# Kernel optimization log

Hardware: AMD Instinct MI355X
Metric: run time of the kernel (lower is better)

Reference implementation:

```python
import jax, jax.numpy as jnp
import numpy as np

D, M, B, K = 512, 128, 16, 4
COHERENCE_COEFF = 0.01
LAMBDA_COEFF = 1.0


def setup_inputs() -> dict:
    key = jax.random.key(0)
    k1, k2, k3, k4 = jax.random.split(key, 4)
    x = jax.random.normal(k1, (2, 2048, D), dtype=jnp.float32)
    V = jax.random.normal(k2, (D, M, B), dtype=jnp.float32)
    U = jax.random.normal(k3, (M, D, B), dtype=jnp.float32)
    u_scales = jax.random.normal(k4, (M, B), dtype=jnp.float32)
    return {"x": x, "V": V, "U": U, "u_scales": u_scales}


def _forward(x, V, U, u_scales):
    # UnitColNorm parametrizations: normalize over the D axis
    Vn = V / jnp.linalg.norm(V, axis=0, keepdims=True)          # (D, m, b)
    Un = U / jnp.linalg.norm(U, axis=1, keepdims=True)          # (m, D, b)
    s = jnp.tanh(u_scales) * LAMBDA_COEFF                        # (m, b)
    U_eff = Un * s[:, None, :]                                   # (m, D, b)

    expert_reprs = jnp.einsum('...d,dmb->...mb', x, Vn)          # (..., m, b)
    repr_l2_sq = jnp.sum(expert_reprs * expert_reprs, axis=-1)   # (..., m)
    topk_vals, topk_idxs = jax.lax.top_k(repr_l2_sq, K)          # (..., k)

    reprs_topk = jnp.take_along_axis(expert_reprs, topk_idxs[..., None], axis=-2)  # (..., k, b)
    U_active = U_eff[topk_idxs]                                  # (..., k, D, b)
    writes = jnp.einsum('...kdb,...kb->...d', U_active, reprs_topk)

    # aux terms
    N = topk_vals.size // K
    idxs_flat = topk_idxs.reshape(-1)
    vals_flat = topk_vals.reshape(-1)
    energy_per_expert = jnp.zeros((M,), dtype=vals_flat.dtype).at[idxs_flat].add(vals_flat) / N
    select_rate = jnp.zeros((M,), dtype=vals_flat.dtype).at[idxs_flat].add(1.0) / N
    total_energy = jnp.maximum(energy_per_expert.sum(), 1e-12)
    relative_energy = energy_per_expert / total_energy

    eye = jnp.eye(M * B, dtype=Vn.dtype)
    sqrtD = jnp.sqrt(jnp.asarray(D, dtype=Vn.dtype))

    def coherence_penalty(Mtx):
        G = Mtx.T @ Mtx  # (m*b, m*b)
        return jnp.abs(G - eye).mean() * sqrtD

    v_pen = coherence_penalty(Vn.reshape(D, M * B))
    u_pen = coherence_penalty(U_eff.transpose(1, 0, 2).reshape(D, M * B))
    aux_loss = COHERENCE_COEFF * v_pen - total_energy

    out = x + writes
    return (out, total_energy, energy_per_expert, relative_energy,
            select_rate, v_pen, u_pen, aux_loss)


def reference(x, V, U, u_scales):
    return _forward(x, V, U, u_scales)
```

## Files before the change

### kernel.cpp

```cpp
#include <hip/hip_runtime.h>
#include <math.h>

#define D 512
#define M 128
#define B 16
#define KSEL 4
#define NC 2048
#define NTOK 4096

typedef unsigned short ushort;
typedef unsigned int uint;
typedef unsigned long long u64;
typedef __attribute__((ext_vector_type(8))) short short8;
typedef __attribute__((ext_vector_type(4))) float floatx4;

#define WS_EACC   0
#define WS_CACC   128
#define WS_VSUM   256
#define WS_USUM   257
#define WS_CNT_I  258
#define WS_VSCALE 512
#define WS_USCALE 2560
#define WS_E_F    4608
#define WS_RBF_F  528896
#define WS_XH_F   2626048
#define WS_XL_F   3674624
#define WS_VHT_F  4723200
#define WS_VLT_F  5247488
#define WS_UHT_F  5771776
#define WS_ULT_F  6296064
#define WS_LIST_F 6820352
#define WS_SEL_F  7344640

#define OUT_TE   2097152
#define OUT_EPE  2097153
#define OUT_RE   2097281
#define OUT_SR   2097409
#define OUT_VPEN 2097537
#define OUT_UPEN 2097538
#define OUT_AUX  2097539

#define GLDS16(g, l) __builtin_amdgcn_global_load_lds(                        \
    (const __attribute__((address_space(1))) unsigned int*)(g),               \
    (__attribute__((address_space(3))) unsigned int*)(l), 16, 0, 0)

__device__ __forceinline__ ushort f2bf(float f) {
    union { float f; uint u; } a; a.f = f;
    uint u = a.u;
    u += 0x7fffu + ((u >> 16) & 1u);
    return (ushort)(u >> 16);
}
__device__ __forceinline__ float bf2f(ushort h) {
    union { uint u; float f; } a; a.u = ((uint)h) << 16;
    return a.f;
}

__launch_bounds__(256)
__global__ void prep_kernel(const float* __restrict__ x, const float* __restrict__ V,
                            const float* __restrict__ U, const float* __restrict__ us_in,
                            ushort* __restrict__ xh, ushort* __restrict__ xl,
                            ushort* __restrict__ vht, ushort* __restrict__ vlt,
                            ushort* __restrict__ uht, ushort* __restrict__ ult,
                            float* __restrict__ ws) {
    __shared__ float ts[64][65];
    const int bid = blockIdx.x;
    const int tid = threadIdx.x;

    if (bid < 1024) {
        const int idx = (bid * 256 + tid) * 8;
        float4 v0 = *(const float4*)(x + idx);
        float4 v1 = *(const float4*)(x + idx + 4);
        float vv[8] = {v0.x, v0.y, v0.z, v0.w, v1.x, v1.y, v1.z, v1.w};
        union { ushort u[8]; uint4 q; } H, L;
#pragma unroll
        for (int j = 0; j < 8; ++j) {
            ushort h = f2bf(vv[j]);
            H.u[j] = h;
            L.u[j] = f2bf(vv[j] - bf2f(h));
        }
        *(uint4*)(xh + idx) = H.q;
        *(uint4*)(xl + idx) = L.q;
    } else if (bid < 1280) {
        const int vb = bid - 1024;
        const int col0 = (vb & 31) * 64;
        const int d0 = (vb >> 5) * 64;
#pragma unroll
        for (int i = 0; i < 16; ++i) {
            int idx = i * 256 + tid;
            int r = idx >> 6, c = idx & 63;
            ts[r][c] = V[(size_t)(d0 + r) * NC + col0 + c];
        }
        __syncthreads();
#pragma unroll
        for (int i = 0; i < 16; ++i) {
            int idx = i * 256 + tid;
            int c2 = idx >> 6, d2 = idx & 63;
            float v = ts[d2][c2];
            ushort h = f2bf(v);
            vht[(size_t)(col0 + c2) * D + d0 + d2] = h;
            vlt[(size_t)(col0 + c2) * D + d0 + d2] = f2bf(v - bf2f(h));
        }
    } else if (bid < 1408) {
        const int m = bid - 1280;
        float (*t2)[129] = (float (*)[129])ts;
        for (int d0 = 0; d0 < D; d0 += 128) {
            __syncthreads();
#pragma unroll
            for (int i = 0; i < 8; ++i) {
                int idx = i * 256 + tid;
                int d2 = idx >> 4, b2 = idx & 15;
                t2[b2][d2] = U[(size_t)m * (D * B) + (size_t)(d0 + d2) * B + b2];
            }
            __syncthreads();
#pragma unroll
            for (int i = 0; i < 8; ++i) {
                int idx = i * 256 + tid;
                int b3 = idx >> 7, d3 = idx & 127;
                uht[(size_t)((m << 4) + b3) * D + d0 + d3] = f2bf(t2[b3][d3]);
            }
        }
    } else {
        const int bx = bid - 1408;
        if (bx >= 160) {
            ws[(bx - 160) * 256 + tid] = 0.0f;
            return;
        }
        if (bx < 32) {
            const int c = bx * 64 + (tid & 63);
            const int dg = tid >> 6;
            float s = 0.0f;
            for (int d = dg; d < D; d += 4) {
                float v = V[(size_t)d * NC + c];
                s = fmaf(v, v, s);
            }
            float (*sh)[64] = (float (*)[64])ts;
            sh[dg][tid & 63] = s;
            __syncthreads();
            if (tid < 64) {
                float t = (sh[0][tid] + sh[1][tid]) + (sh[2][tid] + sh[3][tid]);
                ws[WS_VSCALE + bx * 64 + tid] = 1.0f / sqrtf(t);
            }
        } else {
            const int m = bx - 32;
            const float* p = U + (size_t)m * (D * B);
            float s = 0.0f;
            for (int i = tid; i < D * B; i += 256) {
                float v = p[i];
                s = fmaf(v, v, s);
            }
            float* sh2 = &ts[0][0];
            sh2[tid] = s;
            __syncthreads();
            if (tid < 16) {
                float t = 0.0f;
#pragma unroll
                for (int j = 0; j < 16; ++j) t += sh2[tid + (j << 4)];
                ws[WS_USCALE + (m << 4) + tid] = tanhf(us_in[(m << 4) + tid]) / sqrtf(t);
            }
        }
    }
}

__launch_bounds__(256)
__global__ void mfma_fused(const ushort* __restrict__ xh, const ushort* __restrict__ xl,
                           const ushort* __restrict__ vht, const ushort* __restrict__ vlt,
                           const ushort* __restrict__ uht, const ushort* __restrict__ ult,
                           float* __restrict__ ws, ushort* __restrict__ rbf) {
    __shared__ ushort smem[16384];
    const int bid = blockIdx.x;
    const int tid = threadIdx.x, lane = tid & 63, w = tid >> 6;
    const int wr = w >> 1, wc = w & 1;
    const int r15 = lane & 15, q = lane >> 4;
    const int srl = lane >> 2;
    const int skq = (lane & 3) ^ ((lane >> 3) & 3);
    const int perm8 = (q ^ ((r15 >> 1) & 3)) * 8;

    const int is_gemm = bid < 512;
    const ushort* srcs[4];
    int rbase[4];
    int gi = 0, gj = 0, which = 0;
    if (is_gemm) {
        const int x = bid & 7, inner = bid >> 3;
        const int tokG = ((x >> 1) << 3) + (inner & 7);
        const int colG = ((x & 1) << 3) + (inner >> 3);
        const int tokB = tokG * 128, colB = colG * 128;
        srcs[0] = xh; srcs[1] = xl; srcs[2] = vht; srcs[3] = vlt;
        rbase[0] = tokB; rbase[1] = tokB; rbase[2] = colB; rbase[3] = colB;
    } else {
        int t = bid - 512;
        which = t >= 136;
        if (which) t -= 136;
        int bi = 0, rem = 16;
        while (t >= rem) { t -= rem; --rem; ++bi; }
        gi = bi; gj = bi + t;
        const ushort* ht = which ? uht : vht;
        srcs[0] = ht; srcs[1] = ht; srcs[2] = ht; srcs[3] = ht;
        rbase[0] = gi * 128; rbase[1] = gi * 128; rbase[2] = gj * 128; rbase[3] = gj * 128;
    }

    floatx4 acc[4][4];
#pragma unroll
    for (int i = 0; i < 4; ++i)
#pragma unroll
        for (int j = 0; j < 4; ++j) acc[i][j] = (floatx4){0.f, 0.f, 0.f, 0.f};

    auto stage = [&](int c) {
        const int kb = c * 32 + skq * 8;
#pragma unroll
        for (int tI = 0; tI < 4; ++tI) {
            if (!is_gemm && (tI & 1)) continue;
            const ushort* s = srcs[tI] + (size_t)rbase[tI] * D + kb;
#pragma unroll
            for (int sub = 0; sub < 2; ++sub) {
                const int row16 = w * 32 + sub * 16;
                GLDS16(s + (size_t)(row16 + srl) * D,
                       &smem[tI * 4096 + row16 * 32]);
            }
        }
    };

    stage(0);
    for (int c = 0; c < 16; ++c) {
        __syncthreads();
        short8 ah[4], al[4], bh[4], bl[4];
#pragma unroll
        for (int s = 0; s < 4; ++s) {
            const int ra = (wr * 64 + s * 16 + r15) * 32 + perm8;
            ah[s] = *(const short8*)&smem[ra];
            const int rb = (wc * 64 + s * 16 + r15) * 32 + perm8;
            bh[s] = *(const short8*)&smem[8192 + rb];
            if (is_gemm) {
                al[s] = *(const short8*)&smem[4096 + ra];
                bl[s] = *(const short8*)&smem[12288 + rb];
            }
        }
        __syncthreads();
        if (c < 15) stage(c + 1);
#pragma unroll
        for (int st = 0; st < 4; ++st)
#pragma unroll
            for (int sc = 0; sc < 4; ++sc) {
                acc[st][sc] = __builtin_amdgcn_mfma_f32_16x16x32_bf16(ah[st], bh[sc], acc[st][sc], 0, 0, 0);
                if (is_gemm) {
                    acc[st][sc] = __builtin_amdgcn_mfma_f32_16x16x32_bf16(ah[st], bl[sc], acc[st][sc], 0, 0, 0);
                    acc[st][sc] = __builtin_amdgcn_mfma_f32_16x16x32_bf16(al[st], bh[sc], acc[st][sc], 0, 0, 0);
                }
            }
    }

    if (is_gemm) {
        const int tok0 = rbase[0] + wr * 64, col0 = rbase[2] + wc * 64;
        const int cg4 = col0 >> 6;
        float* e2base = ws + WS_E_F + (size_t)cg4 * (NTOK * 4);
#pragma unroll
        for (int st = 0; st < 4; ++st) {
            const int rowb = tok0 + st * 16 + q * 4;
            float er[4][4];
#pragma unroll
            for (int sc = 0; sc < 4; ++sc) {
                const int colg = col0 + sc * 16 + r15;
                const float vs = ws[WS_VSCALE + colg];
                float r0 = acc[st][sc][0] * vs;
                float r1 = acc[st][sc][1] * vs;
                float r2 = acc[st][sc][2] * vs;
                float r3 = acc[st][sc][3] * vs;
                rbf[(size_t)(rowb + 0) * NC + colg] = f2bf(r0);
                rbf[(size_t)(rowb + 1) * NC + colg] = f2bf(r1);
                rbf[(size_t)(rowb + 2) * NC + colg] = f2bf(r2);
                rbf[(size_t)(rowb + 3) * NC + colg] = f2bf(r3);
                float e0 = r0 * r0, e1 = r1 * r1, e2 = r2 * r2, e3 = r3 * r3;
#pragma unroll
                for (int mk = 1; mk < 16; mk <<= 1) {
                    e0 += __shfl_xor(e0, mk);
                    e1 += __shfl_xor(e1, mk);
                    e2 += __shfl_xor(e2, mk);
                    e3 += __shfl_xor(e3, mk);
                }
                er[sc][0] = e0; er[sc][1] = e1; er[sc][2] = e2; er[sc][3] = e3;
            }
            if (r15 == 0) {
#pragma unroll
                for (int j = 0; j < 4; ++j) {
                    *(float4*)(e2base + (size_t)(rowb + j) * 4) =
                        make_float4(er[0][j], er[1][j], er[2][j], er[3][j]);
                }
            }
        }
    } else {
        const float* scl = ws + (which ? WS_USCALE : WS_VSCALE);
        float* sum_out = ws + (which ? WS_USUM : WS_VSUM);
        float local = 0.0f;
#pragma unroll
        for (int sc = 0; sc < 4; ++sc) {
            const int colg = gj * 128 + wc * 64 + sc * 16 + r15;
            const float scj = scl[colg];
#pragma unroll
            for (int st = 0; st < 4; ++st) {
#pragma unroll
                for (int reg = 0; reg < 4; ++reg) {
                    const int rowg = gi * 128 + wr * 64 + st * 16 + q * 4 + reg;
                    float g = acc[st][sc][reg] * scl[rowg] * scj;
                    if (rowg == colg) g -= 1.0f;
                    local += fabsf(g);
                }
            }
        }
        if (gi < gj) local *= 2.0f;
#pragma unroll
        for (int mk = 1; mk < 64; mk <<= 1) local += __shfl_xor(local, mk);
        __shared__ float red[4];
        if (lane == 0) red[w] = local;
        __syncthreads();
        if (tid == 0) atomicAdd(sum_out, (red[0] + red[1]) + (red[2] + red[3]));
    }
}

__launch_bounds__(256)
__global__ void topk_kernel(float* __restrict__ ws) {
    const int tid = threadIdx.x, lane = tid & 63, w = tid >> 6;
    const int t = blockIdx.x * 4 + w;

    const int cg4 = lane >> 1;
    const int e2off = (lane & 1) * 2;
    const float2 ev = *(const float2*)(ws + WS_E_F +
                                       ((size_t)cg4 * NTOK + t) * 4 + e2off);
    const uint i0 = (uint)(lane * 2), i1 = i0 + 1;
    u64 k0 = ((u64)__float_as_uint(ev.x) << 32) | (uint)(~i0);
    u64 k1 = ((u64)__float_as_uint(ev.y) << 32) | (uint)(~i1);
    u64 s0 = k0 > k1 ? k0 : k1;
    u64 s1 = k0 > k1 ? k1 : k0;
    u64 s2 = 0, s3 = 0;

#pragma unroll
    for (int mk = 1; mk < 64; mk <<= 1) {
        u64 o0 = __shfl_xor(s0, mk);
        u64 o1 = __shfl_xor(s1, mk);
        u64 o2 = __shfl_xor(s2, mk);
        u64 o3 = __shfl_xor(s3, mk);
        u64 c0 = s0 > o3 ? s0 : o3;
        u64 c1 = s1 > o2 ? s1 : o2;
        u64 c2 = s2 > o1 ? s2 : o1;
        u64 c3 = s3 > o0 ? s3 : o0;
        u64 d0 = c0 > c2 ? c0 : c2, d2 = c0 > c2 ? c2 : c0;
        u64 d1 = c1 > c3 ? c1 : c3, d3 = c1 > c3 ? c3 : c1;
        s0 = d0 > d1 ? d0 : d1; s1 = d0 > d1 ? d1 : d0;
        s2 = d2 > d3 ? d2 : d3; s3 = d2 > d3 ? d3 : d2;
    }

    if (lane < 4) {
        u64 key = (lane == 0) ? s0 : (lane == 1) ? s1 : (lane == 2) ? s2 : s3;
        const uint e = (uint)(~(uint)key) & 127u;
        const u64 lo = ((u64)(e << 14)) | (u64)((t << 2) | lane);
        ((u64*)(ws + WS_SEL_F))[(t << 2) + lane] =
            (key & 0xFFFFFFFF00000000ull) | lo;
    }
}

__launch_bounds__(256)
__global__ void listbuild_kernel(float* __restrict__ ws) {
    const int e = blockIdx.x;
    const int tid = threadIdx.x;
    const u64* sels = (const u64*)(ws + WS_SEL_F);
    int* icnt = (int*)ws + WS_CNT_I;
    int* ilist = (int*)(ws + WS_LIST_F) + (e << 12);

    __shared__ int sc_[256];
    __shared__ float sv[256];

    const int base_idx = tid * 64;
    int cnt = 0;
    float vsum = 0.0f;
#pragma unroll 8
    for (int j = 0; j < 64; ++j) {
        u64 s = sels[base_idx + j];
        if ((int)((s >> 14) & 127u) == e) {
            ++cnt;
            vsum += __uint_as_float((uint)(s >> 32));
        }
    }
    sc_[tid] = cnt;
    sv[tid] = vsum;
    __syncthreads();

#pragma unroll
    for (int off = 1; off < 256; off <<= 1) {
        int v = (tid >= off) ? sc_[tid - off] : 0;
        __syncthreads();
        sc_[tid] += v;
        __syncthreads();
    }
    const int wbase = sc_[tid] - cnt;
    const int total = sc_[255];

    if (cnt > 0) {
        int p = wbase;
#pragma unroll 8
        for (int j = 0; j < 64; ++j) {
            u64 s = sels[base_idx + j];
            if ((int)((s >> 14) & 127u) == e)
                ilist[p++] = (int)(s & 0x3FFFu);
        }
    }

#pragma unroll
    for (int off = 128; off > 0; off >>= 1) {
        __syncthreads();
        if (tid < off) sv[tid] += sv[tid + off];
    }
    if (tid == 0) {
        icnt[e] = total;
        ws[WS_EACC + e] = sv[0];
        ws[WS_CACC + e] = (float)total;
    }
}

__launch_bounds__(256)
__global__ void expert_contrib_kernel(const float* __restrict__ U,
                                      const ushort* __restrict__ rbf,
                                      const float* __restrict__ ws,
                                      uint* __restrict__ contrib) {
    const int e = blockIdx.x;
    const int tid = threadIdx.x;
    const int cnt = ((const int*)ws)[WS_CNT_I + e];
    if ((int)blockIdx.y >= cnt) return;

    float usc[16];
#pragma unroll
    for (int b = 0; b < 16; ++b) usc[b] = ws[WS_USCALE + (e << 4) + b];

    const float* Up = U + (size_t)e * (D * B);
    float u0[16], u1[16];
#pragma unroll
    for (int qd = 0; qd < 4; ++qd) {
        float4 a = *(const float4*)(Up + (size_t)(2 * tid) * B + qd * 4);
        float4 b4 = *(const float4*)(Up + (size_t)(2 * tid + 1) * B + qd * 4);
        u0[qd * 4 + 0] = a.x * usc[qd * 4 + 0];
        u0[qd * 4 + 1] = a.y * usc[qd * 4 + 1];
        u0[qd * 4 + 2] = a.z * usc[qd * 4 + 2];
        u0[qd * 4 + 3] = a.w * usc[qd * 4 + 3];
        u1[qd * 4 + 0] = b4.x * usc[qd * 4 + 0];
        u1[qd * 4 + 1] = b4.y * usc[qd * 4 + 1];
        u1[qd * 4 + 2] = b4.z * usc[qd * 4 + 2];
        u1[qd * 4 + 3] = b4.w * usc[qd * 4 + 3];
    }

    const int* ilist = (const int*)(ws + WS_LIST_F) + (e << 12);
    int i = blockIdx.y;
    int pk = (i < cnt) ? ilist[i] : 0;
    while (i < cnt) {
        const int t = pk >> 2, k = pk & 3;
        const ushort* rp = rbf + (size_t)t * NC + (e << 4);
        union { ushort u[16]; uint4 q[2]; } R;
        R.q[0] = *(const uint4*)(rp);
        R.q[1] = *(const uint4*)(rp + 8);
        const int inext = i + 8;
        if (inext < cnt) pk = ilist[inext];
        float acc0 = 0.0f, acc1 = 0.0f;
#pragma unroll
        for (int b = 0; b < 16; ++b) {
            const float wv = bf2f(R.u[b]);
            acc0 = fmaf(u0[b], wv, acc0);
            acc1 = fmaf(u1[b], wv, acc1);
        }
        contrib[(size_t)((t << 2) + k) * 256 + tid] =
            (uint)f2bf(acc0) | ((uint)f2bf(acc1) << 16);
        i = inext;
    }
}

__launch_bounds__(256)
__global__ void combine_kernel(const float* __restrict__ x,
                               const uint* __restrict__ contrib,
                               const float* __restrict__ ws,
                               float* __restrict__ out) {
    if (blockIdx.x == 1024) {
        const int m = threadIdx.x;
        if (m >= 128) return;
        float e = ws[WS_EACC + m] * (1.0f / (float)NTOK);
        float c = ws[WS_CACC + m] * (1.0f / (float)NTOK);
        float s = e;
#pragma unroll
        for (int off = 32; off > 0; off >>= 1) s += __shfl_down(s, off);
        __shared__ float sh[2];
        if ((m & 63) == 0) sh[m >> 6] = s;
        __syncthreads();
        float total = sh[0] + sh[1];
        float total_energy = fmaxf(total, 1e-12f);
        out[OUT_EPE + m] = e;
        out[OUT_RE + m] = e / total_energy;
        out[OUT_SR + m] = c;
        if (m == 0) {
            out[OUT_TE] = total_energy;
            float inv_n2 = 1.0f / ((float)NC * (float)NC);
            float sqrtD = sqrtf((float)D);
            float vpen = ws[WS_VSUM] * inv_n2 * sqrtD;
            float upen = ws[WS_USUM] * inv_n2 * sqrtD;
            out[OUT_VPEN] = vpen;
            out[OUT_UPEN] = upen;
            out[OUT_AUX] = 0.01f * vpen - total_energy;
        }
        return;
    }

    const int gid = blockIdx.x * 256 + threadIdx.x;
    const int t = gid >> 6;
    const int dq = (gid & 63) << 3;
    const uint4* cp = (const uint4*)contrib;

    float s[8];
    float4 x0 = *(const float4*)(x + (size_t)t * D + dq);
    float4 x1 = *(const float4*)(x + (size_t)t * D + dq + 4);
    s[0] = x0.x; s[1] = x0.y; s[2] = x0.z; s[3] = x0.w;
    s[4] = x1.x; s[5] = x1.y; s[6] = x1.z; s[7] = x1.w;
#pragma unroll
    for (int k = 0; k < KSEL; ++k) {
        uint4 cvec = cp[(size_t)((t << 2) + k) * 64 + (dq >> 3)];
        uint cc[4] = {cvec.x, cvec.y, cvec.z, cvec.w};
#pragma unroll
        for (int j = 0; j < 4; ++j) {
            s[2 * j]     += bf2f((ushort)(cc[j] & 0xffffu));
            s[2 * j + 1] += bf2f((ushort)(cc[j] >> 16));
        }
    }
    float* op = out + (size_t)t * D + dq;
    *(float4*)(op)     = make_float4(s[0], s[1], s[2], s[3]);
    *(float4*)(op + 4) = make_float4(s[4], s[5], s[6], s[7]);
}

extern "C" void kernel_launch(void* const* d_in, const int* in_sizes, int n_in,
                              void* d_out, int out_size, void* d_ws, size_t ws_size,
                              hipStream_t stream) {
    const float* x  = (const float*)d_in[0];
    const float* V  = (const float*)d_in[1];
    const float* U  = (const float*)d_in[2];
    const float* us = (const float*)d_in[3];
    float* out = (float*)d_out;
    float* ws  = (float*)d_ws;

    ushort* xh  = (ushort*)(ws + WS_XH_F);
    ushort* xl  = (ushort*)(ws + WS_XL_F);
    ushort* vht = (ushort*)(ws + WS_VHT_F);
    ushort* vlt = (ushort*)(ws + WS_VLT_F);
    ushort* uht = (ushort*)(ws + WS_UHT_F);
    ushort* ult = (ushort*)(ws + WS_ULT_F);
    ushort* rbf = (ushort*)(ws + WS_RBF_F);
    uint* contrib = (uint*)(ws + WS_XH_F);

    prep_kernel<<<1570, 256, 0, stream>>>(x, V, U, us, xh, xl, vht, vlt, uht, ult, ws);
    mfma_fused<<<784, 256, 0, stream>>>(xh, xl, vht, vlt, uht, ult, ws, rbf);
    topk_kernel<<<NTOK / 4, 256, 0, stream>>>(ws);
    listbuild_kernel<<<M, 256, 0, stream>>>(ws);
    expert_contrib_kernel<<<dim3(128, 8), 256, 0, stream>>>(U, rbf, ws, contrib);
    combine_kernel<<<1025, 256, 0, stream>>>(x, contrib, ws, out);
}
```

Before: 168.9 us.

## Fuse topk, list build, expert contrib and combine into one cooperative kernel

The four tail kernels (top-k selection, per-expert list build, expert contribution, final combine) are merged into one cooperatively launched kernel of 1024 blocks, with grid-wide syncs between phases. The aim is to remove the launch gaps and drain/fill bubbles between these small kernels. The cost is three grid barriers. It also requires all 1024 blocks to be co-resident, which `__launch_bounds__(256, 4)` targets. Unused `ult` pointer arguments are dropped from the earlier kernels.

```diff
diff --git a/kernel.cpp b/kernel.cpp
--- a/kernel.cpp
+++ b/kernel.cpp
@@ -1,5 +1,8 @@
 #include <hip/hip_runtime.h>
+#include <hip/hip_cooperative_groups.h>
 #include <math.h>
+
+namespace cg = cooperative_groups;
 
 #define D 512
 #define M 128
@@ -60,7 +63,7 @@
                             const float* __restrict__ U, const float* __restrict__ us_in,
                             ushort* __restrict__ xh, ushort* __restrict__ xl,
                             ushort* __restrict__ vht, ushort* __restrict__ vlt,
-                            ushort* __restrict__ uht, ushort* __restrict__ ult,
+                            ushort* __restrict__ uht,
                             float* __restrict__ ws) {
     __shared__ float ts[64][65];
     const int bid = blockIdx.x;
@@ -164,7 +167,7 @@
 __launch_bounds__(256)
 __global__ void mfma_fused(const ushort* __restrict__ xh, const ushort* __restrict__ xl,
                            const ushort* __restrict__ vht, const ushort* __restrict__ vlt,
-                           const ushort* __restrict__ uht, const ushort* __restrict__ ult,
+                           const ushort* __restrict__ uht,
                            float* __restrict__ ws, ushort* __restrict__ rbf) {
     __shared__ ushort smem[16384];
     const int bid = blockIdx.x;
@@ -315,216 +318,218 @@
     }
 }
 
-__launch_bounds__(256)
-__global__ void topk_kernel(float* __restrict__ ws) {
+__launch_bounds__(256, 4)
+__global__ void tail_kernel(const float* __restrict__ x, const float* __restrict__ U,
+                            const ushort* __restrict__ rbf, float* __restrict__ ws,
+                            uint* __restrict__ contrib, float* __restrict__ out) {
+    cg::grid_group grid = cg::this_grid();
+    const int bid = blockIdx.x;
     const int tid = threadIdx.x, lane = tid & 63, w = tid >> 6;
-    const int t = blockIdx.x * 4 + w;
-
-    const int cg4 = lane >> 1;
-    const int e2off = (lane & 1) * 2;
-    const float2 ev = *(const float2*)(ws + WS_E_F +
-                                       ((size_t)cg4 * NTOK + t) * 4 + e2off);
-    const uint i0 = (uint)(lane * 2), i1 = i0 + 1;
-    u64 k0 = ((u64)__float_as_uint(ev.x) << 32) | (uint)(~i0);
-    u64 k1 = ((u64)__float_as_uint(ev.y) << 32) | (uint)(~i1);
-    u64 s0 = k0 > k1 ? k0 : k1;
-    u64 s1 = k0 > k1 ? k1 : k0;
-    u64 s2 = 0, s3 = 0;
-
-#pragma unroll
-    for (int mk = 1; mk < 64; mk <<= 1) {
-        u64 o0 = __shfl_xor(s0, mk);
-        u64 o1 = __shfl_xor(s1, mk);
-        u64 o2 = __shfl_xor(s2, mk);
-        u64 o3 = __shfl_xor(s3, mk);
-        u64 c0 = s0 > o3 ? s0 : o3;
-        u64 c1 = s1 > o2 ? s1 : o2;
-        u64 c2 = s2 > o1 ? s2 : o1;
-        u64 c3 = s3 > o0 ? s3 : o0;
-        u64 d0 = c0 > c2 ? c0 : c2, d2 = c0 > c2 ? c2 : c0;
-        u64 d1 = c1 > c3 ? c1 : c3, d3 = c1 > c3 ? c3 : c1;
-        s0 = d0 > d1 ? d0 : d1; s1 = d0 > d1 ? d1 : d0;
-        s2 = d2 > d3 ? d2 : d3; s3 = d2 > d3 ? d3 : d2;
-    }
-
-    if (lane < 4) {
-        u64 key = (lane == 0) ? s0 : (lane == 1) ? s1 : (lane == 2) ? s2 : s3;
-        const uint e = (uint)(~(uint)key) & 127u;
-        const u64 lo = ((u64)(e << 14)) | (u64)((t << 2) | lane);
-        ((u64*)(ws + WS_SEL_F))[(t << 2) + lane] =
-            (key & 0xFFFFFFFF00000000ull) | lo;
-    }
-}
-
-__launch_bounds__(256)
-__global__ void listbuild_kernel(float* __restrict__ ws) {
-    const int e = blockIdx.x;
-    const int tid = threadIdx.x;
-    const u64* sels = (const u64*)(ws + WS_SEL_F);
-    int* icnt = (int*)ws + WS_CNT_I;
-    int* ilist = (int*)(ws + WS_LIST_F) + (e << 12);
 
     __shared__ int sc_[256];
     __shared__ float sv[256];
-
-    const int base_idx = tid * 64;
-    int cnt = 0;
-    float vsum = 0.0f;
-#pragma unroll 8
-    for (int j = 0; j < 64; ++j) {
-        u64 s = sels[base_idx + j];
-        if ((int)((s >> 14) & 127u) == e) {
-            ++cnt;
-            vsum += __uint_as_float((uint)(s >> 32));
-        }
-    }
-    sc_[tid] = cnt;
-    sv[tid] = vsum;
-    __syncthreads();
-
-#pragma unroll
-    for (int off = 1; off < 256; off <<= 1) {
-        int v = (tid >= off) ? sc_[tid - off] : 0;
-        __syncthreads();
-        sc_[tid] += v;
-        __syncthreads();
-    }
-    const int wbase = sc_[tid] - cnt;
-    const int total = sc_[255];
-
-    if (cnt > 0) {
-        int p = wbase;
+    __shared__ float sh2[2];
+
+    {
+        const int t = bid * 4 + w;
+        const int cg4 = lane >> 1;
+        const int e2off = (lane & 1) * 2;
+        const float2 ev = *(const float2*)(ws + WS_E_F +
+                                           ((size_t)cg4 * NTOK + t) * 4 + e2off);
+        const uint i0 = (uint)(lane * 2), i1 = i0 + 1;
+        u64 k0 = ((u64)__float_as_uint(ev.x) << 32) | (uint)(~i0);
+        u64 k1 = ((u64)__float_as_uint(ev.y) << 32) | (uint)(~i1);
+        u64 s0 = k0 > k1 ? k0 : k1;
+        u64 s1 = k0 > k1 ? k1 : k0;
+        u64 s2 = 0, s3 = 0;
+
+#pragma unroll
+        for (int mk = 1; mk < 64; mk <<= 1) {
+            u64 o0 = __shfl_xor(s0, mk);
+            u64 o1 = __shfl_xor(s1, mk);
+            u64 o2 = __shfl_xor(s2, mk);
+            u64 o3 = __shfl_xor(s3, mk);
+            u64 c0 = s0 > o3 ? s0 : o3;
+            u64 c1 = s1 > o2 ? s1 : o2;
+            u64 c2 = s2 > o1 ? s2 : o1;
+            u64 c3 = s3 > o0 ? s3 : o0;
+            u64 d0 = c0 > c2 ? c0 : c2, d2 = c0 > c2 ? c2 : c0;
+            u64 d1 = c1 > c3 ? c1 : c3, d3 = c1 > c3 ? c3 : c1;
+            s0 = d0 > d1 ? d0 : d1; s1 = d0 > d1 ? d1 : d0;
+            s2 = d2 > d3 ? d2 : d3; s3 = d2 > d3 ? d3 : d2;
+        }
+
+        if (lane < 4) {
+            u64 key = (lane == 0) ? s0 : (lane == 1) ? s1 : (lane == 2) ? s2 : s3;
+            const uint e = (uint)(~(uint)key) & 127u;
+            const u64 lo = ((u64)(e << 14)) | (u64)((t << 2) | lane);
+            ((u64*)(ws + WS_SEL_F))[(t << 2) + lane] =
+                (key & 0xFFFFFFFF00000000ull) | lo;
+        }
+    }
+    grid.sync();
+
+    if (bid < M) {
+        const int e = bid;
+        const u64* sels = (const u64*)(ws + WS_SEL_F);
+        int* icnt = (int*)ws + WS_CNT_I;
+        int* ilist = (int*)(ws + WS_LIST_F) + (e << 12);
+
+        const int base_idx = tid * 64;
+        int cnt = 0;
+        float vsum = 0.0f;
 #pragma unroll 8
         for (int j = 0; j < 64; ++j) {
             u64 s = sels[base_idx + j];
-            if ((int)((s >> 14) & 127u) == e)
-                ilist[p++] = (int)(s & 0x3FFFu);
-        }
-    }
-
-#pragma unroll
-    for (int off = 128; off > 0; off >>= 1) {
+            if ((int)((s >> 14) & 127u) == e) {
+                ++cnt;
+                vsum += __uint_as_float((uint)(s >> 32));
+            }
+        }
+        sc_[tid] = cnt;
+        sv[tid] = vsum;
         __syncthreads();
-        if (tid < off) sv[tid] += sv[tid + off];
-    }
-    if (tid == 0) {
-        icnt[e] = total;
-        ws[WS_EACC + e] = sv[0];
-        ws[WS_CACC + e] = (float)total;
-    }
-}
-
-__launch_bounds__(256)
-__global__ void expert_contrib_kernel(const float* __restrict__ U,
-                                      const ushort* __restrict__ rbf,
-                                      const float* __restrict__ ws,
-                                      uint* __restrict__ contrib) {
-    const int e = blockIdx.x;
-    const int tid = threadIdx.x;
-    const int cnt = ((const int*)ws)[WS_CNT_I + e];
-    if ((int)blockIdx.y >= cnt) return;
-
-    float usc[16];
-#pragma unroll
-    for (int b = 0; b < 16; ++b) usc[b] = ws[WS_USCALE + (e << 4) + b];
-
-    const float* Up = U + (size_t)e * (D * B);
-    float u0[16], u1[16];
-#pragma unroll
-    for (int qd = 0; qd < 4; ++qd) {
-        float4 a = *(const float4*)(Up + (size_t)(2 * tid) * B + qd * 4);
-        float4 b4 = *(const float4*)(Up + (size_t)(2 * tid + 1) * B + qd * 4);
-        u0[qd * 4 + 0] = a.x * usc[qd * 4 + 0];
-        u0[qd * 4 + 1] = a.y * usc[qd * 4 + 1];
-        u0[qd * 4 + 2] = a.z * usc[qd * 4 + 2];
-        u0[qd * 4 + 3] = a.w * usc[qd * 4 + 3];
-        u1[qd * 4 + 0] = b4.x * usc[qd * 4 + 0];
-        u1[qd * 4 + 1] = b4.y * usc[qd * 4 + 1];
-        u1[qd * 4 + 2] = b4.z * usc[qd * 4 + 2];
-        u1[qd * 4 + 3] = b4.w * usc[qd * 4 + 3];
-    }
-
-    const int* ilist = (const int*)(ws + WS_LIST_F) + (e << 12);
-    int i = blockIdx.y;
-    int pk = (i < cnt) ? ilist[i] : 0;
-    while (i < cnt) {
-        const int t = pk >> 2, k = pk & 3;
-        const ushort* rp = rbf + (size_t)t * NC + (e << 4);
-        union { ushort u[16]; uint4 q[2]; } R;
-        R.q[0] = *(const uint4*)(rp);
-        R.q[1] = *(const uint4*)(rp + 8);
-        const int inext = i + 8;
-        if (inext < cnt) pk = ilist[inext];
-        float acc0 = 0.0f, acc1 = 0.0f;
-#pragma unroll
-        for (int b = 0; b < 16; ++b) {
-            const float wv = bf2f(R.u[b]);
-            acc0 = fmaf(u0[b], wv, acc0);
-            acc1 = fmaf(u1[b], wv, acc1);
-        }
-        contrib[(size_t)((t << 2) + k) * 256 + tid] =
-            (uint)f2bf(acc0) | ((uint)f2bf(acc1) << 16);
-        i = inext;
-    }
-}
-
-__launch_bounds__(256)
-__global__ void combine_kernel(const float* __restrict__ x,
-                               const uint* __restrict__ contrib,
-                               const float* __restrict__ ws,
-                               float* __restrict__ out) {
-    if (blockIdx.x == 1024) {
-        const int m = threadIdx.x;
-        if (m >= 128) return;
-        float e = ws[WS_EACC + m] * (1.0f / (float)NTOK);
-        float c = ws[WS_CACC + m] * (1.0f / (float)NTOK);
+
+#pragma unroll
+        for (int off = 1; off < 256; off <<= 1) {
+            int v = (tid >= off) ? sc_[tid - off] : 0;
+            __syncthreads();
+            sc_[tid] += v;
+            __syncthreads();
+        }
+        const int wbase = sc_[tid] - cnt;
+        const int total = sc_[255];
+
+        if (cnt > 0) {
+            int p = wbase;
+#pragma unroll 8
+            for (int j = 0; j < 64; ++j) {
+                u64 s = sels[base_idx + j];
+                if ((int)((s >> 14) & 127u) == e)
+                    ilist[p++] = (int)(s & 0x3FFFu);
+            }
+        }
+
+#pragma unroll
+        for (int off = 128; off > 0; off >>= 1) {
+            __syncthreads();
+            if (tid < off) sv[tid] += sv[tid + off];
+        }
+        if (tid == 0) {
+            icnt[e] = total;
+            ws[WS_EACC + e] = sv[0];
+            ws[WS_CACC + e] = (float)total;
+        }
+    }
+    grid.sync();
+
+    {
+        const int e = bid & 127;
+        const int y = bid >> 7;
+        const int cnt = ((const int*)ws)[WS_CNT_I + e];
+        if (y < cnt) {
+            float usc[16];
+#pragma unroll
+            for (int b = 0; b < 16; ++b) usc[b] = ws[WS_USCALE + (e << 4) + b];
+
+            const float* Up = U + (size_t)e * (D * B);
+            float u0[16], u1[16];
+#pragma unroll
+            for (int qd = 0; qd < 4; ++qd) {
+                float4 a = *(const float4*)(Up + (size_t)(2 * tid) * B + qd * 4);
+                float4 b4 = *(const float4*)(Up + (size_t)(2 * tid + 1) * B + qd * 4);
+                u0[qd * 4 + 0] = a.x * usc[qd * 4 + 0];
+                u0[qd * 4 + 1] = a.y * usc[qd * 4 + 1];
+                u0[qd * 4 + 2] = a.z * usc[qd * 4 + 2];
+                u0[qd * 4 + 3] = a.w * usc[qd * 4 + 3];
+                u1[qd * 4 + 0] = b4.x * usc[qd * 4 + 0];
+                u1[qd * 4 + 1] = b4.y * usc[qd * 4 + 1];
+                u1[qd * 4 + 2] = b4.z * usc[qd * 4 + 2];
+                u1[qd * 4 + 3] = b4.w * usc[qd * 4 + 3];
+            }
+
+            const int* ilist = (const int*)(ws + WS_LIST_F) + (e << 12);
+            int i = y;
+            int pk = ilist[i];
+            while (i < cnt) {
+                const int t = pk >> 2, k = pk & 3;
+                const ushort* rp = rbf + (size_t)t * NC + (e << 4);
+                union { ushort u[16]; uint4 q[2]; } R;
+                R.q[0] = *(const uint4*)(rp);
+                R.q[1] = *(const uint4*)(rp + 8);
+                const int inext = i + 8;
+                if (inext < cnt) pk = ilist[inext];
+                float acc0 = 0.0f, acc1 = 0.0f;
+#pragma unroll
+                for (int b = 0; b < 16; ++b) {
+                    const float wv = bf2f(R.u[b]);
+                    acc0 = fmaf(u0[b], wv, acc0);
+                    acc1 = fmaf(u1[b], wv, acc1);
+                }
+                contrib[(size_t)((t << 2) + k) * 256 + tid] =
+                    (uint)f2bf(acc0) | ((uint)f2bf(acc1) << 16);
+                i = inext;
+            }
+        }
+    }
+    grid.sync();
+
+    if (bid == 0) {
+        const int m = tid;
+        float e = 0.0f, c = 0.0f;
+        if (m < 128) {
+            e = ws[WS_EACC + m] * (1.0f / (float)NTOK);
+            c = ws[WS_CACC + m] * (1.0f / (float)NTOK);
+        }
         float s = e;
 #pragma unroll
         for (int off = 32; off > 0; off >>= 1) s += __shfl_down(s, off);
-        __shared__ float sh[2];
-        if ((m & 63) == 0) sh[m >> 6] = s;
+        if (m == 0) sh2[0] = s;
+        if (m == 64) sh2[1] = s;
         __syncthreads();
-        float total = sh[0] + sh[1];
-        float total_energy = fmaxf(total, 1e-12f);
-        out[OUT_EPE + m] = e;
-        out[OUT_RE + m] = e / total_energy;
-        out[OUT_SR + m] = c;
-        if (m == 0) {
-            out[OUT_TE] = total_energy;
-            float inv_n2 = 1.0f / ((float)NC * (float)NC);
-            float sqrtD = sqrtf((float)D);
-            float vpen = ws[WS_VSUM] * inv_n2 * sqrtD;
-            float upen = ws[WS_USUM] * inv_n2 * sqrtD;
-            out[OUT_VPEN] = vpen;
-            out[OUT_UPEN] = upen;
-            out[OUT_AUX] = 0.01f * vpen - total_energy;
-        }
-        return;
-    }
-
-    const int gid = blockIdx.x * 256 + threadIdx.x;
-    const int t = gid >> 6;
-    const int dq = (gid & 63) << 3;
-    const uint4* cp = (const uint4*)contrib;
-
-    float s[8];
-    float4 x0 = *(const float4*)(x + (size_t)t * D + dq);
-    float4 x1 = *(const float4*)(x + (size_t)t * D + dq + 4);
-    s[0] = x0.x; s[1] = x0.y; s[2] = x0.z; s[3] = x0.w;
-    s[4] = x1.x; s[5] = x1.y; s[6] = x1.z; s[7] = x1.w;
-#pragma unroll
-    for (int k = 0; k < KSEL; ++k) {
-        uint4 cvec = cp[(size_t)((t << 2) + k) * 64 + (dq >> 3)];
-        uint cc[4] = {cvec.x, cvec.y, cvec.z, cvec.w};
-#pragma unroll
-        for (int j = 0; j < 4; ++j) {
-            s[2 * j]     += bf2f((ushort)(cc[j] & 0xffffu));
-            s[2 * j + 1] += bf2f((ushort)(cc[j] >> 16));
-        }
-    }
-    float* op = out + (size_t)t * D + dq;
-    *(float4*)(op)     = make_float4(s[0], s[1], s[2], s[3]);
-    *(float4*)(op + 4) = make_float4(s[4], s[5], s[6], s[7]);
+        if (m < 128) {
+            float total = sh2[0] + sh2[1];
+            float total_energy = fmaxf(total, 1e-12f);
+            out[OUT_EPE + m] = e;
+            out[OUT_RE + m] = e / total_energy;
+            out[OUT_SR + m] = c;
+            if (m == 0) {
+                out[OUT_TE] = total_energy;
+                float inv_n2 = 1.0f / ((float)NC * (float)NC);
+                float sqrtD = sqrtf((float)D);
+                float vpen = ws[WS_VSUM] * inv_n2 * sqrtD;
+                float upen = ws[WS_USUM] * inv_n2 * sqrtD;
+                out[OUT_VPEN] = vpen;
+                out[OUT_UPEN] = upen;
+                out[OUT_AUX] = 0.01f * vpen - total_energy;
+            }
+        }
+    }
+    {
+        const int gid = bid * 256 + tid;
+        const int t = gid >> 6;
+        const int dq = (gid & 63) << 3;
+        const uint4* cp = (const uint4*)contrib;
+
+        float s[8];
+        float4 x0 = *(const float4*)(x + (size_t)t * D + dq);
+        float4 x1 = *(const float4*)(x + (size_t)t * D + dq + 4);
+        s[0] = x0.x; s[1] = x0.y; s[2] = x0.z; s[3] = x0.w;
+        s[4] = x1.x; s[5] = x1.y; s[6] = x1.z; s[7] = x1.w;
+#pragma unroll
+        for (int k = 0; k < KSEL; ++k) {
+            uint4 cvec = cp[(size_t)((t << 2) + k) * 64 + (dq >> 3)];
+            uint cc[4] = {cvec.x, cvec.y, cvec.z, cvec.w};
+#pragma unroll
+            for (int j = 0; j < 4; ++j) {
+                s[2 * j]     += bf2f((ushort)(cc[j] & 0xffffu));
+                s[2 * j + 1] += bf2f((ushort)(cc[j] >> 16));
+            }
+        }
+        float* op = out + (size_t)t * D + dq;
+        *(float4*)(op)     = make_float4(s[0], s[1], s[2], s[3]);
+        *(float4*)(op + 4) = make_float4(s[4], s[5], s[6], s[7]);
+    }
 }
 
 extern "C" void kernel_launch(void* const* d_in, const int* in_sizes, int n_in,
@@ -542,14 +547,15 @@
     ushort* vht = (ushort*)(ws + WS_VHT_F);
     ushort* vlt = (ushort*)(ws + WS_VLT_F);
     ushort* uht = (ushort*)(ws + WS_UHT_F);
-    ushort* ult = (ushort*)(ws + WS_ULT_F);
     ushort* rbf = (ushort*)(ws + WS_RBF_F);
     uint* contrib = (uint*)(ws + WS_XH_F);
 
-    prep_kernel<<<1570, 256, 0, stream>>>(x, V, U, us, xh, xl, vht, vlt, uht, ult, ws);
-    mfma_fused<<<784, 256, 0, stream>>>(xh, xl, vht, vlt, uht, ult, ws, rbf);
-    topk_kernel<<<NTOK / 4, 256, 0, stream>>>(ws);
-    listbuild_kernel<<<M, 256, 0, stream>>>(ws);
-    expert_contrib_kernel<<<dim3(128, 8), 256, 0, stream>>>(U, rbf, ws, contrib);
-    combine_kernel<<<1025, 256, 0, stream>>>(x, contrib, ws, out);
+    prep_kernel<<<1570, 256, 0, stream>>>(x, V, U, us, xh, xl, vht, vlt, uht, ws);
+    mfma_fused<<<784, 256, 0, stream>>>(xh, xl, vht, vlt, uht, ws, rbf);
+
+    const ushort* rbf_c = rbf;
+    void* args[] = {(void*)&x, (void*)&U, (void*)&rbf_c, (void*)&ws,
+                    (void*)&contrib, (void*)&out};
+    hipLaunchCooperativeKernel((void*)tail_kernel, dim3(1024), dim3(256),
+                               args, 0, stream);
 }
```

New measurement: 439.2 us. +160.1%, slower.
